# Kernel tuning notes

Hardware: AMD Instinct MI355X
Metric: run time of the kernel (lower is better)

Reference implementation:

```python
import jax, jax.numpy as jnp
import numpy as np

NOT_EPSILON = 1.0

def swishmax(x, axis):
    # x * exp(x - max) normalized by sum(|.|) + 1 over `axis`
    xexp = x * jnp.exp(x - jnp.max(x, axis=axis, keepdims=True))
    return xexp / (jnp.sum(jnp.abs(xexp), axis=axis, keepdims=True) + NOT_EPSILON)

def setup_inputs() -> dict:
    key = jax.random.key(0)
    ks = jax.random.split(key, 8)
    B, S, D = 2, 512, 256
    std = 0.02
    x = jax.random.normal(ks[0], (B, S, D), dtype=jnp.float32)
    w_pre = jax.random.normal(ks[1], (D, D), dtype=jnp.float32) * std
    w_q   = jax.random.normal(ks[2], (D, D), dtype=jnp.float32) * std
    w_k   = jax.random.normal(ks[3], (D, D), dtype=jnp.float32) * std
    w_va  = jax.random.normal(ks[4], (D, D), dtype=jnp.float32) * std
    w_al  = jax.random.normal(ks[5], (D, D), dtype=jnp.float32) * std
    w_vo  = jax.random.normal(ks[6], (D, D), dtype=jnp.float32) * std
    w_end = jax.random.normal(ks[7], (D, D), dtype=jnp.float32) * std
    return {"x": x, "w_pre": w_pre, "w_q": w_q, "w_k": w_k,
            "w_va": w_va, "w_al": w_al, "w_vo": w_vo, "w_end": w_end}

def reference(x, w_pre, w_q, w_k, w_va, w_al, w_vo, w_end):
    # pre: module_1d = Linear(D, D, bias=False)
    X = x @ w_pre.T                                    # [B,S,D]
    # FractalAttention depth=2 (base case): row_dims=(-3,)
    q = X + X @ w_q.T                                  # residual query proj
    k = X + X @ w_k.T                                  # residual key proj
    # batchify: key lhs -> [B,Sk,1,D], query rhs -> [B,1,Sq,D]
    raw = k[:, :, None, :] * q[:, None, :, :]          # [B,Sk,Sq,D]
    logits = raw + raw @ w_al.T                        # residual logit proj over D
    scale = swishmax(logits, axis=-3)                  # normalize over Sk
    v = X + X @ w_va.T
    vs = v[:, :, None, :] * scale                      # [B,Sk,Sq,D]
    vsum = jnp.sum(vs, axis=-3)                        # [B,Sq,D]
    vout = vsum + vsum @ w_vo.T
    X = X + vout                                       # transformer residual
    X = X @ w_end.T                                    # end: module_1d
    return X
```

## Files before the change

### kernel.cpp

```cpp
#include <hip/hip_runtime.h>
#include <hip/hip_bf16.h>


typedef __attribute__((ext_vector_type(8))) short short8;
typedef __attribute__((ext_vector_type(4))) float f32x4;
typedef __attribute__((ext_vector_type(4))) unsigned short ushort4v;

#define DD 256
#define SS 512
#define LOG2E 1.4426950408889634f
#define LN2   0.6931471805599453f

__device__ __forceinline__ unsigned short f2bf(float f) {
  unsigned int b = __float_as_uint(f);
  b += 0x7FFFu + ((b >> 16) & 1u);
  return (unsigned short)(b >> 16);
}
__device__ __forceinline__ float bf2f(unsigned short u) {
  return __uint_as_float(((unsigned int)u) << 16);
}
__device__ __forceinline__ short8 cvt8(f32x4 lo, f32x4 hi) {
  short8 r;
  r[0]=(short)f2bf(lo[0]); r[1]=(short)f2bf(lo[1]);
  r[2]=(short)f2bf(lo[2]); r[3]=(short)f2bf(lo[3]);
  r[4]=(short)f2bf(hi[0]); r[5]=(short)f2bf(hi[1]);
  r[6]=(short)f2bf(hi[2]); r[7]=(short)f2bf(hi[3]);
  return r;
}
__device__ __forceinline__ void gload16(const void* g, void* l) {
  __builtin_amdgcn_global_load_lds(
      (const __attribute__((address_space(1))) void*)g,
      (__attribute__((address_space(3))) void*)l,
      16, 0, 0);
}

__global__ __launch_bounds__(256) void prep_weights(
    const float* __restrict__ w0, const float* __restrict__ w1,
    const float* __restrict__ w2, const float* __restrict__ w3,
    const float* __restrict__ w4, const float* __restrict__ w5,
    const float* __restrict__ wal, unsigned short* __restrict__ out)
{
  const int bi = blockIdx.x;
  const int m = bi >> 5;
  const int off = ((bi & 31) * 256 + threadIdx.x) * 8;
  const float* src = m==0?w0: m==1?w1: m==2?w2: m==3?w3: m==4?w4: m==5?w5: wal;
  f32x4 a = *(const f32x4*)(src + off);
  f32x4 b = *(const f32x4*)(src + off + 4);
  if (m == 6) {
    const int e = off >> 8, d = off & 255;
#pragma unroll
    for (int jj = 0; jj < 4; ++jj) {
      if (e == d + jj)     a[jj] += 1.0f;
      if (e == d + 4 + jj) b[jj] += 1.0f;
    }
  }
  *(short8*)(out + (size_t)m * 65536 + off) = cvt8(a, b);
}

__global__ __launch_bounds__(256) void linear_bf(
    const float* __restrict__ A, const unsigned short* __restrict__ Wbf,
    const float* __restrict__ res1, const float* __restrict__ res2,
    float* __restrict__ out)
{
  const int bi = blockIdx.x;
  const int rb = (bi >> 2) * 16;
  const int cb = (bi & 3) * 64;
  const int tid = threadIdx.x;
  const int wv = tid >> 6, lane = tid & 63;
  const int g = lane >> 4, c = lane & 15;
  const int arow = rb + c;
  const int wrow = cb + wv * 16 + c;

  f32x4 acc = (f32x4){0.f, 0.f, 0.f, 0.f};
#pragma unroll
  for (int ks = 0; ks < 8; ++ks) {
    const int d0 = ks * 32 + g * 8;
    f32x4 a0 = *(const f32x4*)(A + arow * DD + d0);
    f32x4 a1 = *(const f32x4*)(A + arow * DD + d0 + 4);
    short8 av = cvt8(a0, a1);
    short8 bv = *(const short8*)(Wbf + wrow * DD + d0);
    acc = __builtin_amdgcn_mfma_f32_16x16x32_bf16(av, bv, acc, 0, 0, 0);
  }
#pragma unroll
  for (int j = 0; j < 4; ++j) {
    const int ro = rb + g * 4 + j;
    const int co = cb + wv * 16 + c;
    float v = acc[j];
    if (res1) v += res1[ro * DD + co];
    if (res2) v += res2[ro * DD + co];
    out[ro * DD + co] = v;
  }
}

__global__ __launch_bounds__(256) void linear_qkv(
    const float* __restrict__ X,
    const unsigned short* __restrict__ Wq, const unsigned short* __restrict__ Wk,
    const unsigned short* __restrict__ Wv,
    float* __restrict__ qout, unsigned short* __restrict__ kout,
    unsigned short* __restrict__ vout)
{
  const int bi = blockIdx.x;
  const int rb = (bi >> 2) * 16;
  const int cb = (bi & 3) * 64;
  const int tid = threadIdx.x;
  const int wv = tid >> 6, lane = tid & 63;
  const int g = lane >> 4, c = lane & 15;
  const int arow = rb + c;
  const int wrow = cb + wv * 16 + c;

  f32x4 aq = (f32x4){0.f,0.f,0.f,0.f};
  f32x4 ak = (f32x4){0.f,0.f,0.f,0.f};
  f32x4 av_ = (f32x4){0.f,0.f,0.f,0.f};
#pragma unroll
  for (int ks = 0; ks < 8; ++ks) {
    const int d0 = ks * 32 + g * 8;
    f32x4 a0 = *(const f32x4*)(X + arow * DD + d0);
    f32x4 a1 = *(const f32x4*)(X + arow * DD + d0 + 4);
    short8 af = cvt8(a0, a1);
    short8 bq = *(const short8*)(Wq + wrow * DD + d0);
    aq = __builtin_amdgcn_mfma_f32_16x16x32_bf16(af, bq, aq, 0, 0, 0);
    short8 bk = *(const short8*)(Wk + wrow * DD + d0);
    ak = __builtin_amdgcn_mfma_f32_16x16x32_bf16(af, bk, ak, 0, 0, 0);
    short8 bv = *(const short8*)(Wv + wrow * DD + d0);
    av_ = __builtin_amdgcn_mfma_f32_16x16x32_bf16(af, bv, av_, 0, 0, 0);
  }
#pragma unroll
  for (int j = 0; j < 4; ++j) {
    const int ro = rb + g * 4 + j;
    const int co = cb + wv * 16 + c;
    const float base = X[ro * DD + co];
    qout[ro * DD + co] = (base + aq[j]) * LOG2E;
    kout[ro * DD + co] = f2bf(base + ak[j]);
    vout[ro * DD + co] = f2bf(base + av_[j]);
  }
}

__global__ __launch_bounds__(512, 4) void fractal_attn(
    const unsigned short* __restrict__ walI,
    const float* __restrict__ q,
    const unsigned short* __restrict__ kbf,
    const unsigned short* __restrict__ vbf,
    float* __restrict__ vsum)
{
  __shared__ char smem[2][32768];

  const int wg = blockIdx.x;
  const int eh = wg & 1;
  const int sq = (wg >> 1) & 511;
  const int b  = wg >> 10;
  const int tid = threadIdx.x;
  const int wv = tid >> 6, lane = tid & 63;
  const int g = lane >> 4, c = lane & 15;

  const unsigned short* kbase = kbf + (size_t)b * SS * DD;
  const unsigned short* vbase = vbf + (size_t)b * SS * DD;
  int srco[2];
#pragma unroll
  for (int it = 0; it < 2; ++it) {
    const int p = it * 512 + tid;
    const int row = p >> 5, gc = p & 31;
    srco[it] = row * DD + (gc ^ (row & 7)) * 8;
  }
  auto stage = [&](int t) {
    char* dst = (char*)smem[t & 1];
    const unsigned short* ks = kbase + t * 32 * DD;
    const unsigned short* vs = vbase + t * 32 * DD;
#pragma unroll
    for (int it = 0; it < 2; ++it) {
      gload16(ks + srco[it], dst + (it * 512 + tid) * 16);
      gload16(vs + srco[it], dst + 16384 + (it * 512 + tid) * 16);
    }
  };

  stage(0);

  short8 afrag[8];
  {
    const float* qrow = q + (size_t)(b * SS + sq) * DD;
    const int e = eh * 128 + wv * 16 + c;
    const unsigned short* wrow = walI + (size_t)e * DD;
#pragma unroll
    for (int ks = 0; ks < 8; ++ks) {
      const int d0 = ks * 32 + g * 8;
      short8 w8 = *(const short8*)(wrow + d0);
      f32x4 q0 = *(const f32x4*)(qrow + d0);
      f32x4 q1 = *(const f32x4*)(qrow + d0 + 4);
      f32x4 lo, hi;
      lo[0] = bf2f((unsigned short)w8[0]) * q0[0];
      lo[1] = bf2f((unsigned short)w8[1]) * q0[1];
      lo[2] = bf2f((unsigned short)w8[2]) * q0[2];
      lo[3] = bf2f((unsigned short)w8[3]) * q0[3];
      hi[0] = bf2f((unsigned short)w8[4]) * q1[0];
      hi[1] = bf2f((unsigned short)w8[5]) * q1[1];
      hi[2] = bf2f((unsigned short)w8[6]) * q1[2];
      hi[3] = bf2f((unsigned short)w8[7]) * q1[3];
      afrag[ks] = cvt8(lo, hi);
    }
  }

  const int cb2 = (c >> 2) & 1;
  int koff[2], voff[2];
#pragma unroll
  for (int n = 0; n < 2; ++n) {
    koff[n] = n * 8192 + c * 512 + ((g ^ (c & 3)) << 4) + (cb2 << 6);
    const int row = n * 16 + c;
    const int g16 = eh * 16 + wv * 2 + (g >> 1);
    voff[n] = 16384 + row * 512 + ((g16 ^ (c & 7)) << 4) + ((g & 1) << 3);
  }

  float mst[4], sst[4], vst[4];
#pragma unroll
  for (int j = 0; j < 4; ++j) { mst[j] = -1e30f; sst[j] = 0.f; vst[j] = 0.f; }

  for (int t = 0; t < 16; ++t) {
    __syncthreads();
    if (t < 15) stage(t + 1);
    const char* kb = (const char*)smem[t & 1];

    f32x4 acc0 = (f32x4){0.f,0.f,0.f,0.f};
    f32x4 acc1 = (f32x4){0.f,0.f,0.f,0.f};
#pragma unroll
    for (int ks = 0; ks < 8; ++ks) {
      short8 b0 = *(const short8*)(kb + (koff[0] ^ (ks << 6)));
      short8 b1 = *(const short8*)(kb + (koff[1] ^ (ks << 6)));
      acc0 = __builtin_amdgcn_mfma_f32_16x16x32_bf16(afrag[ks], b0, acc0, 0, 0, 0);
      acc1 = __builtin_amdgcn_mfma_f32_16x16x32_bf16(afrag[ks], b1, acc1, 0, 0, 0);
    }
    ushort4v vq0 = *(const ushort4v*)(kb + voff[0]);
    ushort4v vq1 = *(const ushort4v*)(kb + voff[1]);

#pragma unroll
    for (int j = 0; j < 4; ++j) {
      const float L0 = acc0[j], L1 = acc1[j];
      mst[j] = fmaxf(mst[j], fmaxf(L0, L1));
      const float e0 = __builtin_amdgcn_exp2f(L0);
      const float e1 = __builtin_amdgcn_exp2f(L1);
      const float p0 = L0 * e0, p1 = L1 * e1;
      sst[j] += fabsf(p0) + fabsf(p1);
      vst[j] = fmaf(bf2f((unsigned short)vq0[j]), p0, vst[j]);
      vst[j] = fmaf(bf2f((unsigned short)vq1[j]), p1, vst[j]);
    }
  }

#pragma unroll
  for (int mask = 1; mask <= 8; mask <<= 1) {
#pragma unroll
    for (int j = 0; j < 4; ++j) {
      mst[j] = fmaxf(mst[j], __shfl_xor(mst[j], mask));
      sst[j] += __shfl_xor(sst[j], mask);
      vst[j] += __shfl_xor(vst[j], mask);
    }
  }

  if (c == 0) {
    float* orow = vsum + (size_t)(b * SS + sq) * DD;
    f32x4 o;
#pragma unroll
    for (int j = 0; j < 4; ++j) {
      const float tt = LN2 * __builtin_amdgcn_exp2f(-mst[j]);
      o[j] = vst[j] * tt / (sst[j] * tt + 1.0f);
    }
    *(f32x4*)(orow + eh * 128 + wv * 16 + g * 4) = o;
  }
}

extern "C" void kernel_launch(void* const* d_in, const int* in_sizes, int n_in,
                              void* d_out, int out_size, void* d_ws, size_t ws_size,
                              hipStream_t stream) {
  const float* x     = (const float*)d_in[0];
  const float* w_pre = (const float*)d_in[1];
  const float* w_q   = (const float*)d_in[2];
  const float* w_k   = (const float*)d_in[3];
  const float* w_va  = (const float*)d_in[4];
  const float* w_al  = (const float*)d_in[5];
  const float* w_vo  = (const float*)d_in[6];
  const float* w_end = (const float*)d_in[7];
  float* out = (float*)d_out;

  char* ws = (char*)d_ws;
  float* X    = (float*)(ws);
  float* q    = (float*)(ws + (1 << 20));
  float* vsum = (float*)(ws + (2 << 20));
  float* Y    = (float*)(ws + (3 << 20));
  unsigned short* k_bf = (unsigned short*)(ws + (4 << 20));
  unsigned short* v_bf = (unsigned short*)(ws + (4 << 20) + (512 << 10));
  unsigned short* wbf  = (unsigned short*)(ws + (5 << 20));

  prep_weights<<<224, 256, 0, stream>>>(w_pre, w_q, w_k, w_va, w_vo, w_end,
                                        w_al, wbf);
  linear_bf<<<256, 256, 0, stream>>>(x, wbf + 0 * 65536, nullptr, nullptr, X);
  linear_qkv<<<256, 256, 0, stream>>>(X, wbf + 1 * 65536, wbf + 2 * 65536,
                                      wbf + 3 * 65536, q, k_bf, v_bf);
  fractal_attn<<<2048, 512, 0, stream>>>(wbf + 6 * 65536, q, k_bf, v_bf, vsum);
  linear_bf<<<256, 256, 0, stream>>>(vsum, wbf + 4 * 65536, vsum, X, Y);
  linear_bf<<<256, 256, 0, stream>>>(Y, wbf + 5 * 65536, nullptr, nullptr, out);
}
```

Measured before the change: 132.2 us.

## Give each attention wave two output tiles and read fp32 V directly from global

```diff
diff --git a/kernel.cpp b/kernel.cpp
--- a/kernel.cpp
+++ b/kernel.cpp
@@ -4,10 +4,10 @@
 
 typedef __attribute__((ext_vector_type(8))) short short8;
 typedef __attribute__((ext_vector_type(4))) float f32x4;
-typedef __attribute__((ext_vector_type(4))) unsigned short ushort4v;
 
 #define DD 256
 #define SS 512
+#define KVB 32
 #define LOG2E 1.4426950408889634f
 #define LN2   0.6931471805599453f
 
@@ -97,7 +97,7 @@
     const unsigned short* __restrict__ Wq, const unsigned short* __restrict__ Wk,
     const unsigned short* __restrict__ Wv,
     float* __restrict__ qout, unsigned short* __restrict__ kout,
-    unsigned short* __restrict__ vout)
+    float* __restrict__ vout)
 {
   const int bi = blockIdx.x;
   const int rb = (bi >> 2) * 16;
@@ -131,18 +131,18 @@
     const float base = X[ro * DD + co];
     qout[ro * DD + co] = (base + aq[j]) * LOG2E;
     kout[ro * DD + co] = f2bf(base + ak[j]);
-    vout[ro * DD + co] = f2bf(base + av_[j]);
-  }
-}
-
-__global__ __launch_bounds__(512, 4) void fractal_attn(
+    vout[ro * DD + co] = base + av_[j];
+  }
+}
+
+__global__ __launch_bounds__(256, 3) void fractal_attn(
     const unsigned short* __restrict__ walI,
     const float* __restrict__ q,
     const unsigned short* __restrict__ kbf,
-    const unsigned short* __restrict__ vbf,
+    const float* __restrict__ vf,
     float* __restrict__ vsum)
 {
-  __shared__ char smem[2][32768];
+  __shared__ char smem[2][16384];
 
   const int wg = blockIdx.x;
   const int eh = wg & 1;
@@ -153,114 +153,140 @@
   const int g = lane >> 4, c = lane & 15;
 
   const unsigned short* kbase = kbf + (size_t)b * SS * DD;
-  const unsigned short* vbase = vbf + (size_t)b * SS * DD;
-  int srco[2];
-#pragma unroll
-  for (int it = 0; it < 2; ++it) {
-    const int p = it * 512 + tid;
+  int srco[4];
+#pragma unroll
+  for (int it = 0; it < 4; ++it) {
+    const int p = it * 256 + tid;
     const int row = p >> 5, gc = p & 31;
     srco[it] = row * DD + (gc ^ (row & 7)) * 8;
   }
   auto stage = [&](int t) {
     char* dst = (char*)smem[t & 1];
-    const unsigned short* ks = kbase + t * 32 * DD;
-    const unsigned short* vs = vbase + t * 32 * DD;
-#pragma unroll
-    for (int it = 0; it < 2; ++it) {
-      gload16(ks + srco[it], dst + (it * 512 + tid) * 16);
-      gload16(vs + srco[it], dst + 16384 + (it * 512 + tid) * 16);
-    }
+    const unsigned short* ks = kbase + t * KVB * DD;
+#pragma unroll
+    for (int it = 0; it < 4; ++it)
+      gload16(ks + srco[it], dst + (it * 256 + tid) * 16);
   };
 
   stage(0);
 
-  short8 afrag[8];
+  short8 afrag[2][8];
   {
     const float* qrow = q + (size_t)(b * SS + sq) * DD;
-    const int e = eh * 128 + wv * 16 + c;
-    const unsigned short* wrow = walI + (size_t)e * DD;
-#pragma unroll
-    for (int ks = 0; ks < 8; ++ks) {
-      const int d0 = ks * 32 + g * 8;
-      short8 w8 = *(const short8*)(wrow + d0);
-      f32x4 q0 = *(const f32x4*)(qrow + d0);
-      f32x4 q1 = *(const f32x4*)(qrow + d0 + 4);
-      f32x4 lo, hi;
-      lo[0] = bf2f((unsigned short)w8[0]) * q0[0];
-      lo[1] = bf2f((unsigned short)w8[1]) * q0[1];
-      lo[2] = bf2f((unsigned short)w8[2]) * q0[2];
-      lo[3] = bf2f((unsigned short)w8[3]) * q0[3];
-      hi[0] = bf2f((unsigned short)w8[4]) * q1[0];
-      hi[1] = bf2f((unsigned short)w8[5]) * q1[1];
-      hi[2] = bf2f((unsigned short)w8[6]) * q1[2];
-      hi[3] = bf2f((unsigned short)w8[7]) * q1[3];
-      afrag[ks] = cvt8(lo, hi);
-    }
-  }
-
-  const int cb2 = (c >> 2) & 1;
-  int koff[2], voff[2];
-#pragma unroll
-  for (int n = 0; n < 2; ++n) {
-    koff[n] = n * 8192 + c * 512 + ((g ^ (c & 3)) << 4) + (cb2 << 6);
-    const int row = n * 16 + c;
-    const int g16 = eh * 16 + wv * 2 + (g >> 1);
-    voff[n] = 16384 + row * 512 + ((g16 ^ (c & 7)) << 4) + ((g & 1) << 3);
-  }
-
-  float mst[4], sst[4], vst[4];
-#pragma unroll
-  for (int j = 0; j < 4; ++j) { mst[j] = -1e30f; sst[j] = 0.f; vst[j] = 0.f; }
+#pragma unroll
+    for (int i = 0; i < 2; ++i) {
+      const int e = eh * 128 + wv * 32 + i * 16 + c;
+      const unsigned short* wrow = walI + (size_t)e * DD;
+#pragma unroll
+      for (int ks = 0; ks < 8; ++ks) {
+        const int d0 = ks * 32 + g * 8;
+        short8 w8 = *(const short8*)(wrow + d0);
+        f32x4 q0 = *(const f32x4*)(qrow + d0);
+        f32x4 q1 = *(const f32x4*)(qrow + d0 + 4);
+        f32x4 lo, hi;
+        lo[0] = bf2f((unsigned short)w8[0]) * q0[0];
+        lo[1] = bf2f((unsigned short)w8[1]) * q0[1];
+        lo[2] = bf2f((unsigned short)w8[2]) * q0[2];
+        lo[3] = bf2f((unsigned short)w8[3]) * q0[3];
+        hi[0] = bf2f((unsigned short)w8[4]) * q1[0];
+        hi[1] = bf2f((unsigned short)w8[5]) * q1[1];
+        hi[2] = bf2f((unsigned short)w8[6]) * q1[2];
+        hi[3] = bf2f((unsigned short)w8[7]) * q1[3];
+        afrag[i][ks] = cvt8(lo, hi);
+      }
+    }
+  }
+
+  const int kbA = c * 512 + ((g ^ (c & 3)) << 4) + (((c >> 2) & 1) << 6);
+  const int kbB = kbA ^ 64;
+
+  const float* vwg = vf + (size_t)b * SS * DD;
+  int voffe[2][2];
+#pragma unroll
+  for (int n = 0; n < 2; ++n)
+#pragma unroll
+    for (int i = 0; i < 2; ++i)
+      voffe[n][i] = (n * 16 + c) * DD + eh * 128 + wv * 32 + i * 16 + g * 4;
+
+  float mst[8], sst[8], vst[8];
+#pragma unroll
+  for (int s = 0; s < 8; ++s) { mst[s] = -1e30f; sst[s] = 0.f; vst[s] = 0.f; }
 
   for (int t = 0; t < 16; ++t) {
     __syncthreads();
+
+    const float* vt = vwg + (size_t)t * KVB * DD;
+    f32x4 vv[2][2];
+#pragma unroll
+    for (int n = 0; n < 2; ++n)
+#pragma unroll
+      for (int i = 0; i < 2; ++i)
+        vv[n][i] = *(const f32x4*)(vt + voffe[n][i]);
     if (t < 15) stage(t + 1);
+
     const char* kb = (const char*)smem[t & 1];
-
-    f32x4 acc0 = (f32x4){0.f,0.f,0.f,0.f};
-    f32x4 acc1 = (f32x4){0.f,0.f,0.f,0.f};
-#pragma unroll
-    for (int ks = 0; ks < 8; ++ks) {
-      short8 b0 = *(const short8*)(kb + (koff[0] ^ (ks << 6)));
-      short8 b1 = *(const short8*)(kb + (koff[1] ^ (ks << 6)));
-      acc0 = __builtin_amdgcn_mfma_f32_16x16x32_bf16(afrag[ks], b0, acc0, 0, 0, 0);
-      acc1 = __builtin_amdgcn_mfma_f32_16x16x32_bf16(afrag[ks], b1, acc1, 0, 0, 0);
-    }
-    ushort4v vq0 = *(const ushort4v*)(kb + voff[0]);
-    ushort4v vq1 = *(const ushort4v*)(kb + voff[1]);
-
-#pragma unroll
-    for (int j = 0; j < 4; ++j) {
-      const float L0 = acc0[j], L1 = acc1[j];
-      mst[j] = fmaxf(mst[j], fmaxf(L0, L1));
-      const float e0 = __builtin_amdgcn_exp2f(L0);
-      const float e1 = __builtin_amdgcn_exp2f(L1);
-      const float p0 = L0 * e0, p1 = L1 * e1;
-      sst[j] += fabsf(p0) + fabsf(p1);
-      vst[j] = fmaf(bf2f((unsigned short)vq0[j]), p0, vst[j]);
-      vst[j] = fmaf(bf2f((unsigned short)vq1[j]), p1, vst[j]);
+    f32x4 acc[2][2];
+#pragma unroll
+    for (int i = 0; i < 2; ++i)
+#pragma unroll
+      for (int n = 0; n < 2; ++n) acc[i][n] = (f32x4){0.f,0.f,0.f,0.f};
+
+#pragma unroll
+    for (int ks2 = 0; ks2 < 4; ++ks2) {
+      short8 bA0 = *(const short8*)(kb + kbA + ks2 * 128);
+      short8 bA1 = *(const short8*)(kb + kbA + ks2 * 128 + 8192);
+      acc[0][0] = __builtin_amdgcn_mfma_f32_16x16x32_bf16(afrag[0][2*ks2], bA0, acc[0][0], 0, 0, 0);
+      acc[1][0] = __builtin_amdgcn_mfma_f32_16x16x32_bf16(afrag[1][2*ks2], bA0, acc[1][0], 0, 0, 0);
+      acc[0][1] = __builtin_amdgcn_mfma_f32_16x16x32_bf16(afrag[0][2*ks2], bA1, acc[0][1], 0, 0, 0);
+      acc[1][1] = __builtin_amdgcn_mfma_f32_16x16x32_bf16(afrag[1][2*ks2], bA1, acc[1][1], 0, 0, 0);
+      short8 bB0 = *(const short8*)(kb + kbB + ks2 * 128);
+      short8 bB1 = *(const short8*)(kb + kbB + ks2 * 128 + 8192);
+      acc[0][0] = __builtin_amdgcn_mfma_f32_16x16x32_bf16(afrag[0][2*ks2+1], bB0, acc[0][0], 0, 0, 0);
+      acc[1][0] = __builtin_amdgcn_mfma_f32_16x16x32_bf16(afrag[1][2*ks2+1], bB0, acc[1][0], 0, 0, 0);
+      acc[0][1] = __builtin_amdgcn_mfma_f32_16x16x32_bf16(afrag[0][2*ks2+1], bB1, acc[0][1], 0, 0, 0);
+      acc[1][1] = __builtin_amdgcn_mfma_f32_16x16x32_bf16(afrag[1][2*ks2+1], bB1, acc[1][1], 0, 0, 0);
+    }
+
+#pragma unroll
+    for (int i = 0; i < 2; ++i) {
+#pragma unroll
+      for (int j = 0; j < 4; ++j) {
+        const int s = i * 4 + j;
+        const float L0 = acc[i][0][j], L1 = acc[i][1][j];
+        mst[s] = fmaxf(fmaxf(mst[s], L0), L1);
+        const float e0 = __builtin_amdgcn_exp2f(L0);
+        const float e1 = __builtin_amdgcn_exp2f(L1);
+        const float p0 = L0 * e0, p1 = L1 * e1;
+        sst[s] += fabsf(p0) + fabsf(p1);
+        vst[s] = fmaf(vv[0][i][j], p0, vst[s]);
+        vst[s] = fmaf(vv[1][i][j], p1, vst[s]);
+      }
     }
   }
 
 #pragma unroll
   for (int mask = 1; mask <= 8; mask <<= 1) {
 #pragma unroll
-    for (int j = 0; j < 4; ++j) {
-      mst[j] = fmaxf(mst[j], __shfl_xor(mst[j], mask));
-      sst[j] += __shfl_xor(sst[j], mask);
-      vst[j] += __shfl_xor(vst[j], mask);
+    for (int s = 0; s < 8; ++s) {
+      mst[s] = fmaxf(mst[s], __shfl_xor(mst[s], mask));
+      sst[s] += __shfl_xor(sst[s], mask);
+      vst[s] += __shfl_xor(vst[s], mask);
     }
   }
 
   if (c == 0) {
     float* orow = vsum + (size_t)(b * SS + sq) * DD;
-    f32x4 o;
-#pragma unroll
-    for (int j = 0; j < 4; ++j) {
-      const float tt = LN2 * __builtin_amdgcn_exp2f(-mst[j]);
-      o[j] = vst[j] * tt / (sst[j] * tt + 1.0f);
-    }
-    *(f32x4*)(orow + eh * 128 + wv * 16 + g * 4) = o;
+#pragma unroll
+    for (int i = 0; i < 2; ++i) {
+      f32x4 o;
+#pragma unroll
+      for (int j = 0; j < 4; ++j) {
+        const int s = i * 4 + j;
+        const float tt = LN2 * __builtin_amdgcn_exp2f(-mst[s]);
+        o[j] = vst[s] * tt / (sst[s] * tt + 1.0f);
+      }
+      *(f32x4*)(orow + eh * 128 + wv * 32 + i * 16 + g * 4) = o;
+    }
   }
 }
 
@@ -283,15 +309,15 @@
   float* vsum = (float*)(ws + (2 << 20));
   float* Y    = (float*)(ws + (3 << 20));
   unsigned short* k_bf = (unsigned short*)(ws + (4 << 20));
-  unsigned short* v_bf = (unsigned short*)(ws + (4 << 20) + (512 << 10));
-  unsigned short* wbf  = (unsigned short*)(ws + (5 << 20));
+  float* v_f32         = (float*)(ws + (4 << 20) + (512 << 10));
+  unsigned short* wbf  = (unsigned short*)(ws + (5 << 20) + (512 << 10));
 
   prep_weights<<<224, 256, 0, stream>>>(w_pre, w_q, w_k, w_va, w_vo, w_end,
                                         w_al, wbf);
   linear_bf<<<256, 256, 0, stream>>>(x, wbf + 0 * 65536, nullptr, nullptr, X);
   linear_qkv<<<256, 256, 0, stream>>>(X, wbf + 1 * 65536, wbf + 2 * 65536,
-                                      wbf + 3 * 65536, q, k_bf, v_bf);
-  fractal_attn<<<2048, 512, 0, stream>>>(wbf + 6 * 65536, q, k_bf, v_bf, vsum);
+                                      wbf + 3 * 65536, q, k_bf, v_f32);
+  fractal_attn<<<2048, 256, 0, stream>>>(wbf + 6 * 65536, q, k_bf, v_f32, vsum);
   linear_bf<<<256, 256, 0, stream>>>(vsum, wbf + 4 * 65536, vsum, X, Y);
   linear_bf<<<256, 256, 0, stream>>>(Y, wbf + 5 * 65536, nullptr, nullptr, out);
 }
```

After: 127.5 us. 3.5% less time.
